# Optimization experiments

Measured on AMD Instinct MI355X. Metric: run time of the kernel, lower is better.

The kernel has to match this reference:

```python
import jax, jax.numpy as jnp
import numpy as np

N, DIM, E, HID = 8192, 1024, 8, 4096


def setup_inputs() -> dict:
    key = jax.random.key(0)
    ks = jax.random.split(key, 7)
    s_in = 1.0 / np.sqrt(DIM)
    s_hid = 1.0 / np.sqrt(HID)
    return {
        "x": jax.random.normal(ks[0], (N, DIM), dtype=jnp.float32),
        "gate_w": jax.random.uniform(ks[1], (DIM, E), jnp.float32, -s_in, s_in),
        "gate_b": jax.random.uniform(ks[2], (E,), jnp.float32, -s_in, s_in),
        "w1": jax.random.uniform(ks[3], (E, DIM, HID), jnp.float32, -s_in, s_in),
        "b1": jax.random.uniform(ks[4], (E, HID), jnp.float32, -s_in, s_in),
        "w2": jax.random.uniform(ks[5], (E, HID, DIM), jnp.float32, -s_hid, s_hid),
        "b2": jax.random.uniform(ks[6], (E, DIM), jnp.float32, -s_hid, s_hid),
    }


def reference(x, gate_w, gate_b, w1, b1, w2, b2):
    # gating: softmax then top-1 (argmax)
    gate_logits = x @ gate_w + gate_b            # [N, E]
    gate_probs = jax.nn.softmax(gate_logits, axis=-1)
    top1 = jnp.argmax(gate_probs, axis=-1)       # [N]
    # dense all-expert FFN, as the original module does
    h = jax.nn.relu(jnp.einsum('nd,edh->neh', x, w1) + b1[None, :, :])   # [N, E, HID]
    expert_out = jnp.einsum('neh,ehd->ned', h, w2) + b2[None, :, :]      # [N, E, DIM]
    # select top-1 expert output per token
    sel = jnp.take_along_axis(expert_out, top1[:, None, None], axis=1)[:, 0, :]  # [N, DIM]
    return sel + x
```

## Files before the change

### kernel.cpp

```cpp
#include <hip/hip_runtime.h>
#include <hip/hip_bf16.h>
#include <stdint.h>

#define N_TOK 8192
#define DIM   1024
#define NEXP  8
#define HID   4096
#define PADROWS 9216

typedef unsigned short u16;
typedef __attribute__((ext_vector_type(8))) short bf16x8;
typedef __attribute__((ext_vector_type(4))) float f32x4;

__device__ inline u16 f2bf(float f) {
  union { float f; uint32_t u; } v; v.f = f;
  uint32_t r = v.u + 0x7fffu + ((v.u >> 16) & 1u);
  return (u16)(r >> 16);
}

__device__ inline void gld_lds16(const void* g, void* lds) {
  __builtin_amdgcn_global_load_lds(
      (const __attribute__((address_space(1))) uint32_t*)g,
      (__attribute__((address_space(3))) uint32_t*)lds, 16, 0, 0);
}


__global__ void zero_kernel(int* counts) {
  if (threadIdx.x < NEXP) counts[threadIdx.x] = 0;
}

__global__ void gate_kernel(const float* __restrict__ x,
                            const float* __restrict__ gw,
                            const float* __restrict__ gb,
                            int* __restrict__ expert_id,
                            int* __restrict__ counts) {
  int wave = threadIdx.x >> 6;
  int lane = threadIdx.x & 63;
  int n = blockIdx.x * 4 + wave;
  const float* xr = x + (size_t)n * DIM;
  float acc[8];
#pragma unroll
  for (int e = 0; e < 8; ++e) acc[e] = 0.f;
  for (int d = lane; d < DIM; d += 64) {
    float xv = xr[d];
    const float4 g0 = *(const float4*)&gw[d * 8];
    const float4 g1 = *(const float4*)&gw[d * 8 + 4];
    acc[0] += xv * g0.x; acc[1] += xv * g0.y;
    acc[2] += xv * g0.z; acc[3] += xv * g0.w;
    acc[4] += xv * g1.x; acc[5] += xv * g1.y;
    acc[6] += xv * g1.z; acc[7] += xv * g1.w;
  }
#pragma unroll
  for (int e = 0; e < 8; ++e)
    for (int off = 32; off > 0; off >>= 1)
      acc[e] += __shfl_xor(acc[e], off);
  if (lane == 0) {
    float best = acc[0] + gb[0];
    int bi = 0;
#pragma unroll
    for (int e = 1; e < 8; ++e) {
      float v = acc[e] + gb[e];
      if (v > best) { best = v; bi = e; }
    }
    expert_id[n] = bi;
    atomicAdd(&counts[bi], 1);
  }
}

__global__ void scan_kernel(const int* __restrict__ counts,
                            int* __restrict__ offs,
                            int* __restrict__ cursor) {
  if (threadIdx.x == 0) {
    int o = 0;
    for (int e = 0; e < NEXP; ++e) {
      offs[e] = o;
      o += (counts[e] + 127) & ~127;
      cursor[e] = 0;
    }
    offs[NEXP] = o;
  }
}

__global__ void gather_kernel(const float* __restrict__ x,
                              const int* __restrict__ expert_id,
                              const int* __restrict__ offs,
                              int* __restrict__ cursor,
                              int* __restrict__ perm,
                              u16* __restrict__ xg) {
  int n = blockIdx.x;
  __shared__ int spos;
  if (threadIdx.x == 0) {
    int e = expert_id[n];
    int p = offs[e] + atomicAdd(&cursor[e], 1);
    perm[p] = n;
    spos = p;
  }
  __syncthreads();
  int pos = spos;
  int i = threadIdx.x * 4;
  const float4 v = *(const float4*)&x[(size_t)n * DIM + i];
  ushort4 o;
  o.x = f2bf(v.x); o.y = f2bf(v.y); o.z = f2bf(v.z); o.w = f2bf(v.w);
  *(ushort4*)&xg[(size_t)pos * DIM + i] = o;
}

__global__ void wconv_kernel(const float* __restrict__ src,
                             u16* __restrict__ dst, int K, int Nc) {
  int e = blockIdx.z;
  int kb = blockIdx.x * 64;
  int nb = blockIdx.y * 64;
  const float* s = src + (size_t)e * K * Nc;
  u16* d = dst + (size_t)e * K * Nc;
  __shared__ u16 tile[64][66];
  int rr = threadIdx.x >> 4;
  int cc = (threadIdx.x & 15) * 4;
#pragma unroll
  for (int p = 0; p < 4; ++p) {
    int row = p * 16 + rr;
    const float4 v = *(const float4*)&s[(size_t)(kb + row) * Nc + nb + cc];
    tile[row][cc + 0] = f2bf(v.x);
    tile[row][cc + 1] = f2bf(v.y);
    tile[row][cc + 2] = f2bf(v.z);
    tile[row][cc + 3] = f2bf(v.w);
  }
  __syncthreads();
#pragma unroll
  for (int p = 0; p < 4; ++p) {
    int n = p * 16 + rr;
    ushort4 o;
    o.x = tile[cc + 0][n];
    o.y = tile[cc + 1][n];
    o.z = tile[cc + 2][n];
    o.w = tile[cc + 3][n];
    *(ushort4*)&d[(size_t)(nb + n) * K + kb + cc] = o;
  }
}


__device__ inline void gemm_core(const u16* __restrict__ Abase,
                                 const u16* __restrict__ Bbase,
                                 int K, f32x4 acc[4][4],
                                 u16* As, u16* Bs) {
  const int tid = threadIdx.x;
  const int wave = tid >> 6, lane = tid & 63;
  const int wr = (wave >> 1) * 64, wc = (wave & 1) * 64;
  const int l15 = lane & 15, l4 = lane >> 4;
  const int srow = lane >> 3;
  const int scol = (lane & 7) * 8;

  for (int kt = 0; kt < K; kt += 64) {
#pragma unroll
    for (int j = 0; j < 4; ++j) {
      int r0 = j * 32 + wave * 8;
      int row = r0 + srow;
      gld_lds16(Abase + (size_t)row * K + kt + scol, &As[r0 * 64]);
      gld_lds16(Bbase + (size_t)row * K + kt + scol, &Bs[r0 * 64]);
    }
    __syncthreads();
#pragma unroll
    for (int ks = 0; ks < 2; ++ks) {
      bf16x8 a[4], b[4];
#pragma unroll
      for (int i = 0; i < 4; ++i)
        a[i] = *(const bf16x8*)&As[(wr + i * 16 + l15) * 64 + ks * 32 + l4 * 8];
#pragma unroll
      for (int i = 0; i < 4; ++i)
        b[i] = *(const bf16x8*)&Bs[(wc + i * 16 + l15) * 64 + ks * 32 + l4 * 8];
#pragma unroll
      for (int mi = 0; mi < 4; ++mi)
#pragma unroll
        for (int ni = 0; ni < 4; ++ni)
          acc[mi][ni] = __builtin_amdgcn_mfma_f32_16x16x32_bf16(
              a[mi], b[ni], acc[mi][ni], 0, 0, 0);
    }
    __syncthreads();
  }
}

__global__ __launch_bounds__(256) void gemm1_kernel(
    const u16* __restrict__ xg, const u16* __restrict__ w1b,
    const float* __restrict__ b1, const int* __restrict__ counts,
    const int* __restrict__ offs, u16* __restrict__ h) {
  int e = blockIdx.z, mt = blockIdx.y, nt = blockIdx.x;
  int ne = counts[e];
  if (mt * 128 >= ne) return;
  int seg = offs[e];
  __shared__ __align__(16) u16 As[128 * 64];
  __shared__ __align__(16) u16 Bs[128 * 64];
  f32x4 acc[4][4];
#pragma unroll
  for (int i = 0; i < 4; ++i)
#pragma unroll
    for (int j = 0; j < 4; ++j) acc[i][j] = (f32x4){0.f, 0.f, 0.f, 0.f};

  const u16* Abase = xg + (size_t)(seg + mt * 128) * DIM;
  const u16* Bbase = w1b + ((size_t)e * HID + nt * 128) * DIM;
  gemm_core(Abase, Bbase, DIM, acc, As, Bs);

  const int tid = threadIdx.x;
  const int wave = tid >> 6, lane = tid & 63;
  const int wr = (wave >> 1) * 64, wc = (wave & 1) * 64;
  const int l15 = lane & 15, l4 = lane >> 4;
  const int rowlim = ne - mt * 128;
  const size_t hrow0 = (size_t)(seg + mt * 128);
#pragma unroll
  for (int mi = 0; mi < 4; ++mi)
#pragma unroll
    for (int j = 0; j < 4; ++j) {
      int r = wr + mi * 16 + l4 * 4 + j;
      if (r < rowlim) {
        u16* hp = h + (hrow0 + r) * (size_t)HID;
#pragma unroll
        for (int ni = 0; ni < 4; ++ni) {
          int c = nt * 128 + wc + ni * 16 + l15;
          float v = acc[mi][ni][j] + b1[e * HID + c];
          hp[c] = f2bf(fmaxf(v, 0.f));
        }
      }
    }
}

__global__ __launch_bounds__(256) void gemm2_kernel(
    const u16* __restrict__ h, const u16* __restrict__ w2b,
    const float* __restrict__ b2, const float* __restrict__ x,
    const int* __restrict__ counts, const int* __restrict__ offs,
    const int* __restrict__ perm, float* __restrict__ out) {
  int e = blockIdx.z, mt = blockIdx.y, nt = blockIdx.x;
  int ne = counts[e];
  if (mt * 128 >= ne) return;
  int seg = offs[e];
  __shared__ __align__(16) u16 As[128 * 64];
  __shared__ __align__(16) u16 Bs[128 * 64];
  f32x4 acc[4][4];
#pragma unroll
  for (int i = 0; i < 4; ++i)
#pragma unroll
    for (int j = 0; j < 4; ++j) acc[i][j] = (f32x4){0.f, 0.f, 0.f, 0.f};

  const u16* Abase = h + (size_t)(seg + mt * 128) * HID;
  const u16* Bbase = w2b + ((size_t)e * DIM + nt * 128) * HID;
  gemm_core(Abase, Bbase, HID, acc, As, Bs);

  const int tid = threadIdx.x;
  const int wave = tid >> 6, lane = tid & 63;
  const int wr = (wave >> 1) * 64, wc = (wave & 1) * 64;
  const int l15 = lane & 15, l4 = lane >> 4;
  const int rowlim = ne - mt * 128;
  const int prow0 = seg + mt * 128;
#pragma unroll
  for (int mi = 0; mi < 4; ++mi)
#pragma unroll
    for (int j = 0; j < 4; ++j) {
      int r = wr + mi * 16 + l4 * 4 + j;
      if (r < rowlim) {
        int orig = perm[prow0 + r];
        const float* xr = x + (size_t)orig * DIM;
        float* op = out + (size_t)orig * DIM;
#pragma unroll
        for (int ni = 0; ni < 4; ++ni) {
          int c = nt * 128 + wc + ni * 16 + l15;
          op[c] = acc[mi][ni][j] + b2[e * DIM + c] + xr[c];
        }
      }
    }
}


extern "C" void kernel_launch(void* const* d_in, const int* in_sizes, int n_in,
                              void* d_out, int out_size, void* d_ws, size_t ws_size,
                              hipStream_t stream) {
  const float* x  = (const float*)d_in[0];
  const float* gw = (const float*)d_in[1];
  const float* gb = (const float*)d_in[2];
  const float* w1 = (const float*)d_in[3];
  const float* b1 = (const float*)d_in[4];
  const float* w2 = (const float*)d_in[5];
  const float* b2 = (const float*)d_in[6];
  float* out = (float*)d_out;

  char* ws = (char*)d_ws;
  int* counts    = (int*)(ws + 0);
  int* offs      = (int*)(ws + 64);
  int* cursor    = (int*)(ws + 128);
  int* expert_id = (int*)(ws + 256);
  int* perm      = (int*)(ws + 33280);
  u16* xg  = (u16*)(ws + (size_t)131072);
  u16* h   = (u16*)(ws + (size_t)0x1400000);
  u16* w1b = (u16*)(ws + (size_t)0x5E00000);
  u16* w2b = (u16*)(ws + (size_t)0x9E00000);

  zero_kernel<<<1, 64, 0, stream>>>(counts);
  gate_kernel<<<N_TOK / 4, 256, 0, stream>>>(x, gw, gb, expert_id, counts);
  scan_kernel<<<1, 64, 0, stream>>>(counts, offs, cursor);
  gather_kernel<<<N_TOK, 256, 0, stream>>>(x, expert_id, offs, cursor, perm, xg);
  wconv_kernel<<<dim3(DIM / 64, HID / 64, NEXP), 256, 0, stream>>>(w1, w1b, DIM, HID);
  wconv_kernel<<<dim3(HID / 64, DIM / 64, NEXP), 256, 0, stream>>>(w2, w2b, HID, DIM);
  gemm1_kernel<<<dim3(HID / 128, N_TOK / 128, NEXP), 256, 0, stream>>>(
      xg, w1b, b1, counts, offs, h);
  gemm2_kernel<<<dim3(DIM / 128, N_TOK / 128, NEXP), 256, 0, stream>>>(
      h, w2b, b2, x, counts, offs, perm, out);
}
```

Before: 908.4 us.

## Double-buffer LDS with XOR swizzle and XCD-aware 1D grid remap in expert GEMMs

Restructures the shared GEMM core into a two-stage LDS ping-pong so global-to-LDS loads of the next K tile overlap MFMA work on the current one, and applies an XOR swizzle to LDS columns to cut bank conflicts. Both GEMM launches become a flat 1D grid whose block index is remapped so consecutive hardware-dispatched blocks (round-robin across XCDs) land on the same expert, improving L2 locality of weights. Launch bounds request two blocks per CU, and the weight-conversion kernel uses vectorized LDS stores. Shared memory per block doubles to 64KB, which may limit occupancy.

```diff
diff --git a/kernel.cpp b/kernel.cpp
--- a/kernel.cpp
+++ b/kernel.cpp
@@ -6,7 +6,9 @@
 #define DIM   1024
 #define NEXP  8
 #define HID   4096
-#define PADROWS 9216
+#define MT_MAX 72
+#define NWG1 (NEXP * MT_MAX * (HID/128))
+#define NWG2 (NEXP * MT_MAX * (DIM/128))
 
 typedef unsigned short u16;
 typedef __attribute__((ext_vector_type(8))) short bf16x8;
@@ -111,17 +113,16 @@
   int nb = blockIdx.y * 64;
   const float* s = src + (size_t)e * K * Nc;
   u16* d = dst + (size_t)e * K * Nc;
-  __shared__ u16 tile[64][66];
+  __shared__ __align__(16) u16 tile[64][68];
   int rr = threadIdx.x >> 4;
   int cc = (threadIdx.x & 15) * 4;
 #pragma unroll
   for (int p = 0; p < 4; ++p) {
     int row = p * 16 + rr;
     const float4 v = *(const float4*)&s[(size_t)(kb + row) * Nc + nb + cc];
-    tile[row][cc + 0] = f2bf(v.x);
-    tile[row][cc + 1] = f2bf(v.y);
-    tile[row][cc + 2] = f2bf(v.z);
-    tile[row][cc + 3] = f2bf(v.w);
+    ushort4 t;
+    t.x = f2bf(v.x); t.y = f2bf(v.y); t.z = f2bf(v.z); t.w = f2bf(v.w);
+    *(ushort4*)&tile[row][cc] = t;
   }
   __syncthreads();
 #pragma unroll
@@ -137,35 +138,42 @@
 }
 
 
-__device__ inline void gemm_core(const u16* __restrict__ Abase,
-                                 const u16* __restrict__ Bbase,
-                                 int K, f32x4 acc[4][4],
-                                 u16* As, u16* Bs) {
+template<int K>
+__device__ __forceinline__ void gemm_core(const u16* __restrict__ Ab,
+                                          const u16* __restrict__ Bb,
+                                          f32x4 acc[4][4], u16* sm) {
   const int tid = threadIdx.x;
   const int wave = tid >> 6, lane = tid & 63;
   const int wr = (wave >> 1) * 64, wc = (wave & 1) * 64;
   const int l15 = lane & 15, l4 = lane >> 4;
   const int srow = lane >> 3;
-  const int scol = (lane & 7) * 8;
-
-  for (int kt = 0; kt < K; kt += 64) {
+  const int schunk = ((lane & 7) ^ srow) * 8;
+
+  u16* A0 = sm;          u16* B0 = sm + 8192;
+  u16* A1 = sm + 16384;  u16* B1 = sm + 24576;
+
+  auto STAGE = [&](u16* Ad, u16* Bd, int kk) {
 #pragma unroll
     for (int j = 0; j < 4; ++j) {
       int r0 = j * 32 + wave * 8;
-      int row = r0 + srow;
-      gld_lds16(Abase + (size_t)row * K + kt + scol, &As[r0 * 64]);
-      gld_lds16(Bbase + (size_t)row * K + kt + scol, &Bs[r0 * 64]);
-    }
-    __syncthreads();
+      gld_lds16(Ab + (size_t)(r0 + srow) * K + kk + schunk, Ad + r0 * 64);
+      gld_lds16(Bb + (size_t)(r0 + srow) * K + kk + schunk, Bd + r0 * 64);
+    }
+  };
+  auto COMPUTE = [&](const u16* As, const u16* Bs) {
 #pragma unroll
     for (int ks = 0; ks < 2; ++ks) {
       bf16x8 a[4], b[4];
 #pragma unroll
-      for (int i = 0; i < 4; ++i)
-        a[i] = *(const bf16x8*)&As[(wr + i * 16 + l15) * 64 + ks * 32 + l4 * 8];
-#pragma unroll
-      for (int i = 0; i < 4; ++i)
-        b[i] = *(const bf16x8*)&Bs[(wc + i * 16 + l15) * 64 + ks * 32 + l4 * 8];
+      for (int i = 0; i < 4; ++i) {
+        int r = wr + i * 16 + l15;
+        a[i] = *(const bf16x8*)&As[r * 64 + ((ks * 32 + l4 * 8) ^ ((r & 7) * 8))];
+      }
+#pragma unroll
+      for (int i = 0; i < 4; ++i) {
+        int r = wc + i * 16 + l15;
+        b[i] = *(const bf16x8*)&Bs[r * 64 + ((ks * 32 + l4 * 8) ^ ((r & 7) * 8))];
+      }
 #pragma unroll
       for (int mi = 0; mi < 4; ++mi)
 #pragma unroll
@@ -173,20 +181,38 @@
           acc[mi][ni] = __builtin_amdgcn_mfma_f32_16x16x32_bf16(
               a[mi], b[ni], acc[mi][ni], 0, 0, 0);
     }
+  };
+
+  constexpr int NST = K / 64;
+  STAGE(A0, B0, 0);
+#pragma unroll 1
+  for (int kt = 0; kt < NST - 2; kt += 2) {
     __syncthreads();
-  }
-}
-
-__global__ __launch_bounds__(256) void gemm1_kernel(
+    STAGE(A1, B1, (kt + 1) * 64);
+    COMPUTE(A0, B0);
+    __syncthreads();
+    STAGE(A0, B0, (kt + 2) * 64);
+    COMPUTE(A1, B1);
+  }
+  __syncthreads();
+  STAGE(A1, B1, (NST - 1) * 64);
+  COMPUTE(A0, B0);
+  __syncthreads();
+  COMPUTE(A1, B1);
+}
+
+__global__ __launch_bounds__(256, 2) void gemm1_kernel(
     const u16* __restrict__ xg, const u16* __restrict__ w1b,
     const float* __restrict__ b1, const int* __restrict__ counts,
     const int* __restrict__ offs, u16* __restrict__ h) {
-  int e = blockIdx.z, mt = blockIdx.y, nt = blockIdx.x;
+  int fid = (int)(blockIdx.x & 7) * (NWG1 / 8) + (int)(blockIdx.x >> 3);
+  int e = fid / (MT_MAX * 32);
+  int rm = fid % (MT_MAX * 32);
+  int mt = rm / 32, nt = rm % 32;
   int ne = counts[e];
   if (mt * 128 >= ne) return;
   int seg = offs[e];
-  __shared__ __align__(16) u16 As[128 * 64];
-  __shared__ __align__(16) u16 Bs[128 * 64];
+  __shared__ __align__(16) u16 sm[32768];
   f32x4 acc[4][4];
 #pragma unroll
   for (int i = 0; i < 4; ++i)
@@ -195,7 +221,7 @@
 
   const u16* Abase = xg + (size_t)(seg + mt * 128) * DIM;
   const u16* Bbase = w1b + ((size_t)e * HID + nt * 128) * DIM;
-  gemm_core(Abase, Bbase, DIM, acc, As, Bs);
+  gemm_core<DIM>(Abase, Bbase, acc, sm);
 
   const int tid = threadIdx.x;
   const int wave = tid >> 6, lane = tid & 63;
@@ -220,17 +246,19 @@
     }
 }
 
-__global__ __launch_bounds__(256) void gemm2_kernel(
+__global__ __launch_bounds__(256, 2) void gemm2_kernel(
     const u16* __restrict__ h, const u16* __restrict__ w2b,
     const float* __restrict__ b2, const float* __restrict__ x,
     const int* __restrict__ counts, const int* __restrict__ offs,
     const int* __restrict__ perm, float* __restrict__ out) {
-  int e = blockIdx.z, mt = blockIdx.y, nt = blockIdx.x;
+  int fid = (int)(blockIdx.x & 7) * (NWG2 / 8) + (int)(blockIdx.x >> 3);
+  int e = fid / (MT_MAX * 8);
+  int rm = fid % (MT_MAX * 8);
+  int mt = rm / 8, nt = rm % 8;
   int ne = counts[e];
   if (mt * 128 >= ne) return;
   int seg = offs[e];
-  __shared__ __align__(16) u16 As[128 * 64];
-  __shared__ __align__(16) u16 Bs[128 * 64];
+  __shared__ __align__(16) u16 sm[32768];
   f32x4 acc[4][4];
 #pragma unroll
   for (int i = 0; i < 4; ++i)
@@ -239,7 +267,7 @@
 
   const u16* Abase = h + (size_t)(seg + mt * 128) * HID;
   const u16* Bbase = w2b + ((size_t)e * DIM + nt * 128) * HID;
-  gemm_core(Abase, Bbase, HID, acc, As, Bs);
+  gemm_core<HID>(Abase, Bbase, acc, sm);
 
   const int tid = threadIdx.x;
   const int wave = tid >> 6, lane = tid & 63;
@@ -295,8 +323,6 @@
   gather_kernel<<<N_TOK, 256, 0, stream>>>(x, expert_id, offs, cursor, perm, xg);
   wconv_kernel<<<dim3(DIM / 64, HID / 64, NEXP), 256, 0, stream>>>(w1, w1b, DIM, HID);
   wconv_kernel<<<dim3(HID / 64, DIM / 64, NEXP), 256, 0, stream>>>(w2, w2b, HID, DIM);
-  gemm1_kernel<<<dim3(HID / 128, N_TOK / 128, NEXP), 256, 0, stream>>>(
-      xg, w1b, b1, counts, offs, h);
-  gemm2_kernel<<<dim3(DIM / 128, N_TOK / 128, NEXP), 256, 0, stream>>>(
-      h, w2b, b2, x, counts, offs, perm, out);
-}
+  gemm1_kernel<<<NWG1, 256, 0, stream>>>(xg, w1b, b1, counts, offs, h);
+  gemm2_kernel<<<NWG2, 256, 0, stream>>>(h, w2b, b2, x, counts, offs, perm, out);
+}
```

Measured after the change: 791.0 us. 12.9% less time.
